# Kernel tuning notes

Measured on AMD Instinct MI355X. Metric: run time of the kernel, lower is better.

## Reference

```python
import jax, jax.numpy as jnp
import numpy as np
from jax.scipy.special import logsumexp

N_STATES = 512
N_OBS = 1024
BATCH = 64
T_MAX = 512


def setup_inputs() -> dict:
    key = jax.random.key(0)
    k1, k2, k3, k4, k5 = jax.random.split(key, 5)
    pi = jnp.zeros((N_STATES,), dtype=jnp.float32)
    A = jax.random.normal(k1, (N_STATES, N_STATES), dtype=jnp.float32)  # unnormalized transition
    E = jax.random.normal(k2, (N_STATES, N_OBS), dtype=jnp.float32)     # unnormalized emission
    x = jax.random.randint(k3, (BATCH, T_MAX), 0, N_OBS)
    T = jax.random.randint(k4, (BATCH,), 1, T_MAX + 1)
    return {"pi": pi, "A": A, "E": E, "x": x, "T": T}


def reference(pi, A, E, x, T):
    # log p(x) via forward algorithm in log domain.
    log_pi = jax.nn.log_softmax(pi)                # (N,)
    log_A = jax.nn.log_softmax(A, axis=0)          # (N,N), matches torch dim=0
    log_E = jax.nn.log_softmax(E, axis=1)          # (N,M)

    # emission log-probs per timestep: (B, T_max, N)
    log_em = jnp.moveaxis(log_E[:, x], 0, -1)

    alpha0 = log_em[:, 0, :] + log_pi              # (B,N)

    def step(carry, em_t):
        # carry: (B,N) over k; log_A: (N_i, N_k)
        # next[b,i] = em_t[b,i] + logsumexp_k(log_A[i,k] + carry[b,k])
        nxt = em_t + logsumexp(log_A[None, :, :] + carry[:, None, :], axis=2)
        return nxt, nxt

    em_rest = jnp.swapaxes(log_em[:, 1:, :], 0, 1)  # (T_max-1, B, N)
    _, alphas = jax.lax.scan(step, alpha0, em_rest)
    log_alpha = jnp.concatenate([alpha0[:, None, :], jnp.swapaxes(alphas, 0, 1)], axis=1)  # (B,T_max,N)

    log_sums = logsumexp(log_alpha, axis=2)         # (B, T_max)
    log_probs = jnp.take_along_axis(log_sums, (T - 1)[:, None], axis=1)  # (B,1)
    return log_probs
```

## Files before the change

kernel.cpp:

```cpp
#include <hip/hip_runtime.h>
#include <math.h>

#define NS   512
#define NO   1024
#define NB   64
#define TMAX 512

#define QREG 48
#define QLDS 16

typedef _Float16 h2v __attribute__((ext_vector_type(2)));

__device__ inline float wave_red_sum(float x) {
#pragma unroll
  for (int o = 32; o; o >>= 1) x += __shfl_xor(x, o, 64);
  return x;
}
__device__ inline float wave_red_max(float x) {
#pragma unroll
  for (int o = 32; o; o >>= 1) x = fmaxf(x, __shfl_xor(x, o, 64));
  return x;
}

__device__ inline float dot2u(unsigned int a, unsigned int b, float c) {
#if __has_builtin(__builtin_amdgcn_fdot2)
  return __builtin_amdgcn_fdot2(__builtin_bit_cast(h2v, a),
                                __builtin_bit_cast(h2v, b), c, false);
#else
  h2v av = __builtin_bit_cast(h2v, a), bv = __builtin_bit_cast(h2v, b);
  return c + (float)av.x * (float)bv.x + (float)av.y * (float)bv.y;
#endif
}

__global__ void k_pi(const float* __restrict__ pi, float* __restrict__ pi_sm) {
  __shared__ float red[8];
  int tid = threadIdx.x;
  float v = pi[tid];
  float m = wave_red_max(v);
  if ((tid & 63) == 0) red[tid >> 6] = m;
  __syncthreads();
  m = fmaxf(fmaxf(fmaxf(red[0], red[1]), fmaxf(red[2], red[3])),
            fmaxf(fmaxf(red[4], red[5]), fmaxf(red[6], red[7])));
  float e = __expf(v - m);
  float s = wave_red_sum(e);
  __syncthreads();
  if ((tid & 63) == 0) red[tid >> 6] = s;
  __syncthreads();
  s = red[0] + red[1] + red[2] + red[3] + red[4] + red[5] + red[6] + red[7];
  pi_sm[tid] = e / s;
}

__global__ void k_colLse(const float* __restrict__ A, float* __restrict__ lseA) {
  __shared__ float redm[4];
  __shared__ float reds[4];
  int k = blockIdx.x, tid = threadIdx.x;
  float a0 = A[tid * NS + k], a1 = A[(tid + 256) * NS + k];
  float m = wave_red_max(fmaxf(a0, a1));
  if ((tid & 63) == 0) redm[tid >> 6] = m;
  __syncthreads();
  m = fmaxf(fmaxf(redm[0], redm[1]), fmaxf(redm[2], redm[3]));
  float s = __expf(a0 - m) + __expf(a1 - m);
  s = wave_red_sum(s);
  if ((tid & 63) == 0) reds[tid >> 6] = s;
  __syncthreads();
  s = reds[0] + reds[1] + reds[2] + reds[3];
  if (tid == 0) lseA[k] = m + __logf(s);
}

__global__ void k_rowLseE(const float* __restrict__ E, float* __restrict__ lseE) {
  __shared__ float red[4];
  int i = blockIdx.x, tid = threadIdx.x;
  const float* row = E + i * NO;
  float a0 = row[tid], a1 = row[tid + 256], a2 = row[tid + 512], a3 = row[tid + 768];
  float m = fmaxf(fmaxf(a0, a1), fmaxf(a2, a3));
  m = wave_red_max(m);
  if ((tid & 63) == 0) red[tid >> 6] = m;
  __syncthreads();
  m = fmaxf(fmaxf(red[0], red[1]), fmaxf(red[2], red[3]));
  float s = __expf(a0 - m) + __expf(a1 - m) + __expf(a2 - m) + __expf(a3 - m);
  s = wave_red_sum(s);
  __syncthreads();
  if ((tid & 63) == 0) red[tid >> 6] = s;
  __syncthreads();
  s = red[0] + red[1] + red[2] + red[3];
  if (tid == 0) lseE[i] = m + __logf(s);
}

__global__ void k_pack(const float* __restrict__ A, const float* __restrict__ lseA,
                       unsigned int* __restrict__ W) {
  int u = blockIdx.x * 512 + threadIdx.x;
  int h = u & 3;
  int ct = u >> 2;
  int t = ct & 511;
  int c = ct >> 9;
  int j = c >> 3, m = c & 7;
  int w = t >> 6, l = t & 63;
  int i  = 64 * j + l;
  int k0 = 64 * w + 8 * m + 2 * h;
  float e0 = __expf(A[i * NS + k0]     - lseA[k0]);
  float e1 = __expf(A[i * NS + k0 + 1] - lseA[k0 + 1]);
  h2v p;
  p.x = (_Float16)e0;
  p.y = (_Float16)e1;
  W[u] = __builtin_bit_cast(unsigned int, p);
}

__global__ __launch_bounds__(512, 1) void k_fwd(
    const float* __restrict__ E, const int* __restrict__ x,
    const int* __restrict__ Tlen, const float* __restrict__ pi_sm,
    const float* __restrict__ lseE, const uint4* __restrict__ Apk,
    float* __restrict__ out) {
  __shared__ uint4 Alds[QLDS * 512];
  __shared__ float Pf[8 * 512];
  __shared__ uint4 vbuf[2][NS / 8];
  __shared__ int xrow[TMAX];
  __shared__ __align__(16) float red[2][8];
  int b = blockIdx.x, tid = threadIdx.x;
  int w = tid >> 6, l = tid & 63;

  uint4 areg[QREG];
#pragma unroll
  for (int q = 0; q < QREG; q++) areg[q] = Apk[q * 512 + tid];
#pragma unroll
  for (int q = 0; q < QLDS; q++) Alds[q * 512 + tid] = Apk[(QREG + q) * 512 + tid];

  for (int t2 = tid; t2 < TMAX; t2 += 512) xrow[t2] = x[b * TMAX + t2];

  float pi_i  = pi_sm[tid];
  float lse_i = lseE[tid];
  const float* Erow = E + tid * NO;
  int Tb = Tlen[b];
  float c = 0.f;
  float Dlog = 0.f;
  int gexp_prev = 19;
  int cur = 0;
  __syncthreads();

  for (int t = 0; t < Tb; t++) {
    int nxt = cur ^ 1;
    float epre = Erow[xrow[t]];
    int gexpw;
    if (t == 0) {
      gexpw = 19;
    } else {
      const float4* rp = (const float4*)red[cur];
      float4 ra = rp[0], rb = rp[1];
      float sp = ((ra.x + ra.y) + (ra.z + ra.w)) + ((rb.x + rb.y) + (rb.z + rb.w));
      float ls = __log2f(sp);
      int e = ((__builtin_bit_cast(int, sp) >> 23) & 0xff) - 126;
      c += ls - Dlog;
      Dlog = (float)gexp_prev + ls;
      gexpw = 19 - gexp_prev - e;
    }
    if (t) {
      const uint4* vp = vbuf[cur];
      uint4 uv0 = vp[8 * w + 0], uv1 = vp[8 * w + 1];
      uint4 uv2 = vp[8 * w + 2], uv3 = vp[8 * w + 3];
      uint4 uv4 = vp[8 * w + 4], uv5 = vp[8 * w + 5];
      uint4 uv6 = vp[8 * w + 6], uv7 = vp[8 * w + 7];
      float acc[8];
#pragma unroll
      for (int j = 0; j < 8; j++) acc[j] = 0.f;
#pragma unroll
      for (int j = 0; j < 8; j++) {
#pragma unroll
        for (int m = 0; m < 8; m++) {
          int cq = j * 8 + m;
          uint4 av = (cq < QREG) ? areg[cq] : Alds[(cq - QREG) * 512 + tid];
          uint4 uv = (m == 0) ? uv0 : (m == 1) ? uv1 : (m == 2) ? uv2 :
                     (m == 3) ? uv3 : (m == 4) ? uv4 : (m == 5) ? uv5 :
                     (m == 6) ? uv6 : uv7;
          acc[j] = dot2u(av.x, uv.x, acc[j]);
          acc[j] = dot2u(av.y, uv.y, acc[j]);
          acc[j] = dot2u(av.z, uv.z, acc[j]);
          acc[j] = dot2u(av.w, uv.w, acc[j]);
        }
      }
#pragma unroll
      for (int j = 0; j < 8; j++) Pf[w * 512 + j * 64 + l] = acc[j];
    }
    __syncthreads();

    {
      float em = __expf(epre - lse_i);
      float raw;
      if (t) {
        float s0 = Pf[tid]          + Pf[512 + tid];
        float s1 = Pf[1024 + tid]   + Pf[1536 + tid];
        float s2 = Pf[2048 + tid]   + Pf[2560 + tid];
        float s3 = Pf[3072 + tid]   + Pf[3584 + tid];
        raw = ((s0 + s1) + (s2 + s3)) * em;
      } else {
        raw = pi_i * em;
      }
      ((_Float16*)vbuf[nxt])[tid] = (_Float16)ldexpf(raw, gexpw);
      float s = wave_red_sum(raw);
      if (l == 0) red[nxt][w] = s;
      gexp_prev = gexpw;
    }
    __syncthreads();
    cur = nxt;
  }
  {
    const float4* rp = (const float4*)red[cur];
    float4 ra = rp[0], rb = rp[1];
    float sp = ((ra.x + ra.y) + (ra.z + ra.w)) + ((rb.x + rb.y) + (rb.z + rb.w));
    c += __log2f(sp) - Dlog;
  }
  if (tid == 0) out[b] = c * 0.69314718055994530942f;
}

extern "C" void kernel_launch(void* const* d_in, const int* in_sizes, int n_in,
                              void* d_out, int out_size, void* d_ws, size_t ws_size,
                              hipStream_t stream) {
  const float* pi = (const float*)d_in[0];
  const float* A  = (const float*)d_in[1];
  const float* E  = (const float*)d_in[2];
  const int*   x  = (const int*)d_in[3];
  const int*   T  = (const int*)d_in[4];
  float* out = (float*)d_out;

  char* ws = (char*)d_ws;
  float*        pi_sm = (float*)(ws + 0);
  float*        lseA  = (float*)(ws + 2048);
  float*        lseE  = (float*)(ws + 4096);
  unsigned int* Apk   = (unsigned int*)(ws + 6144);

  hipLaunchKernelGGL(k_pi,      dim3(1),   dim3(512), 0, stream, pi, pi_sm);
  hipLaunchKernelGGL(k_colLse,  dim3(512), dim3(256), 0, stream, A, lseA);
  hipLaunchKernelGGL(k_rowLseE, dim3(512), dim3(256), 0, stream, E, lseE);
  hipLaunchKernelGGL(k_pack,    dim3(256), dim3(512), 0, stream, A, lseA, Apk);
  hipLaunchKernelGGL(k_fwd,     dim3(64),  dim3(512), 0, stream,
                     E, x, T, pi_sm, lseE, (const uint4*)Apk, out);
}
```

Baseline: 886.5 us.

## Double-buffer partial sums to drop one barrier per forward step

Pf becomes double-buffered and the half-precision state vector moves to a single buffer, which each wave writes and later reads only for its own 64-entry slice. This lets the trailing __syncthreads in each time step be removed, leaving one barrier per recurrence step instead of two. The scale and log-normalizer update moves after the barrier. QREG is raised from 48 to 50 to keep more of A in registers and fewer in LDS, which raises register pressure and risks spills.

```diff
diff --git a/kernel.cpp b/kernel.cpp
--- a/kernel.cpp
+++ b/kernel.cpp
@@ -6,8 +6,8 @@
 #define NB   64
 #define TMAX 512
 
-#define QREG 48
-#define QLDS 16
+#define QREG 50
+#define QLDS 14
 
 typedef _Float16 h2v __attribute__((ext_vector_type(2)));
 
@@ -111,8 +111,8 @@
     const float* __restrict__ lseE, const uint4* __restrict__ Apk,
     float* __restrict__ out) {
   __shared__ uint4 Alds[QLDS * 512];
-  __shared__ float Pf[8 * 512];
-  __shared__ uint4 vbuf[2][NS / 8];
+  __shared__ float Pf[2][8 * 512];
+  __shared__ uint4 ubuf[NS / 8];
   __shared__ int xrow[TMAX];
   __shared__ __align__(16) float red[2][8];
   int b = blockIdx.x, tid = threadIdx.x;
@@ -139,25 +139,11 @@
   for (int t = 0; t < Tb; t++) {
     int nxt = cur ^ 1;
     float epre = Erow[xrow[t]];
-    int gexpw;
-    if (t == 0) {
-      gexpw = 19;
-    } else {
-      const float4* rp = (const float4*)red[cur];
-      float4 ra = rp[0], rb = rp[1];
-      float sp = ((ra.x + ra.y) + (ra.z + ra.w)) + ((rb.x + rb.y) + (rb.z + rb.w));
-      float ls = __log2f(sp);
-      int e = ((__builtin_bit_cast(int, sp) >> 23) & 0xff) - 126;
-      c += ls - Dlog;
-      Dlog = (float)gexp_prev + ls;
-      gexpw = 19 - gexp_prev - e;
-    }
     if (t) {
-      const uint4* vp = vbuf[cur];
-      uint4 uv0 = vp[8 * w + 0], uv1 = vp[8 * w + 1];
-      uint4 uv2 = vp[8 * w + 2], uv3 = vp[8 * w + 3];
-      uint4 uv4 = vp[8 * w + 4], uv5 = vp[8 * w + 5];
-      uint4 uv6 = vp[8 * w + 6], uv7 = vp[8 * w + 7];
+      uint4 uv0 = ubuf[8 * w + 0], uv1 = ubuf[8 * w + 1];
+      uint4 uv2 = ubuf[8 * w + 2], uv3 = ubuf[8 * w + 3];
+      uint4 uv4 = ubuf[8 * w + 4], uv5 = ubuf[8 * w + 5];
+      uint4 uv6 = ubuf[8 * w + 6], uv7 = ubuf[8 * w + 7];
       float acc[8];
 #pragma unroll
       for (int j = 0; j < 8; j++) acc[j] = 0.f;
@@ -177,30 +163,42 @@
         }
       }
 #pragma unroll
-      for (int j = 0; j < 8; j++) Pf[w * 512 + j * 64 + l] = acc[j];
+      for (int j = 0; j < 8; j++) Pf[cur][w * 512 + j * 64 + l] = acc[j];
     }
     __syncthreads();
 
     {
+      int gexpw = 19;
+      if (t) {
+        const float4* rp = (const float4*)red[cur];
+        float4 ra = rp[0], rb = rp[1];
+        float sp = ((ra.x + ra.y) + (ra.z + ra.w)) + ((rb.x + rb.y) + (rb.z + rb.w));
+        float ls = __log2f(sp);
+        int e = ((__builtin_bit_cast(int, sp) >> 23) & 0xff) - 126;
+        c += ls - Dlog;
+        Dlog = (float)gexp_prev + ls;
+        gexpw = 19 - gexp_prev - e;
+      }
       float em = __expf(epre - lse_i);
       float raw;
       if (t) {
-        float s0 = Pf[tid]          + Pf[512 + tid];
-        float s1 = Pf[1024 + tid]   + Pf[1536 + tid];
-        float s2 = Pf[2048 + tid]   + Pf[2560 + tid];
-        float s3 = Pf[3072 + tid]   + Pf[3584 + tid];
+        const float* pf = Pf[cur];
+        float s0 = pf[tid]          + pf[512 + tid];
+        float s1 = pf[1024 + tid]   + pf[1536 + tid];
+        float s2 = pf[2048 + tid]   + pf[2560 + tid];
+        float s3 = pf[3072 + tid]   + pf[3584 + tid];
         raw = ((s0 + s1) + (s2 + s3)) * em;
       } else {
         raw = pi_i * em;
       }
-      ((_Float16*)vbuf[nxt])[tid] = (_Float16)ldexpf(raw, gexpw);
+      ((_Float16*)ubuf)[tid] = (_Float16)ldexpf(raw, gexpw);
       float s = wave_red_sum(raw);
       if (l == 0) red[nxt][w] = s;
       gexp_prev = gexpw;
     }
-    __syncthreads();
     cur = nxt;
   }
+  __syncthreads();
   {
     const float4* rp = (const float4*)red[cur];
     float4 ra = rp[0], rb = rp[1];
```

New measurement: 833.3 us. 6.0% less time.
